# Performance work log

Measured on AMD Instinct MI355X. Metric: run time of the kernel, lower is better.

Reference implementation:

```python
import jax, jax.numpy as jnp
import numpy as np

B, V = 256, 128256

def setup_inputs() -> dict:
    key = jax.random.key(0)
    k1, k2, k3 = jax.random.split(key, 3)
    logits = jax.random.normal(k1, (B, V), dtype=jnp.float32)
    # temperatures in (0, 1.5], with every 8th request greedy (temp == 0)
    u = jax.random.uniform(k2, (B,), dtype=jnp.float32)
    temperatures = jnp.where(jnp.arange(B) % 8 == 0, 0.0, u * 1.4 + 0.1)
    # uniform noise in [0, 1); transformed to Exp(1) inside reference
    noise = jax.random.uniform(k3, (B, V), dtype=jnp.float32)
    return {"logits": logits, "temperatures": temperatures, "noise": noise}

def reference(logits, temperatures, noise):
    logits = logits.astype(jnp.float32)
    greedy_tokens = jnp.argmax(logits, axis=-1)                      # [B]
    scaled = logits / temperatures[:, None]                           # [B, V]
    probs = jax.nn.softmax(scaled, axis=-1)                           # [B, V]
    # torch.empty_like(probs).exponential_(1)  ==  -log(1 - U),  U ~ Uniform[0,1)
    exp_noise = -jnp.log1p(-noise)                                    # Exp(1) noise
    sample_tokens = jnp.argmax(probs / exp_noise, axis=-1)            # Gumbel-max equiv.
    return jnp.where(temperatures == 0, greedy_tokens, sample_tokens)
```

## Files before the change

### kernel.cpp

```cpp
#include <hip/hip_runtime.h>
#include <math.h>


constexpr int TPB = 1024;
constexpr int CHUNKS = 4;

__device__ __forceinline__ void amax_comb(float v, int i, float& bv, int& bi) {
    if (v > bv || (v == bv && i < bi)) { bv = v; bi = i; }
}

__device__ __forceinline__ float gumbel_key(float l, float u, float c) {
    const float w   = 1.0f - u;
    const float enw = __log2f(w) * -0.693147180559945f;
    float p = 0.16666667f;
    p = fmaf(p, u, 0.2f);
    p = fmaf(p, u, 0.25f);
    p = fmaf(p, u, 0.33333333f);
    p = fmaf(p, u, 0.5f);
    p = fmaf(p, u, 1.0f);
    const float en = (u < 0.125f) ? p * u : enw;
    return fmaf(l, c, -__log2f(en));
}

__global__ __launch_bounds__(TPB, 8) void sampler_phase1(
    const float* __restrict__ logits,
    const float* __restrict__ temps,
    const float* __restrict__ noise,
    float* __restrict__ ws_val,
    int* __restrict__ ws_idx, int V)
{
    const int chunk = blockIdx.x & (CHUNKS - 1);
    const int b     = blockIdx.x / CHUNKS;
    const int V4    = V >> 2;
    const int V4c   = V4 / CHUNKS;
    const int gbase = chunk * V4c;
    const float temp = temps[b];
    const float4* __restrict__ lg4 =
        (const float4*)(logits + (size_t)b * V) + gbase;
    const float4* __restrict__ nz4 =
        (const float4*)(noise + (size_t)b * V) + gbase;
    const int t = threadIdx.x;
    const int last = V4c - 1;

    float bv = -INFINITY;
    int   bi = 0x7fffffff;

    if (temp == 0.0f) {
        float4 A = lg4[min(t, last)];
        float4 Bq = lg4[min(t + TPB, last)];
        for (int j = 0; j * TPB < V4c; ++j) {
            const int f = t + j * TPB;
            const float4 l = A;
            A = Bq;
            Bq = lg4[min(f + 2 * TPB, last)];
            if (f < V4c) {
                const int base = (gbase + f) << 2;
                if (l.x > bv) { bv = l.x; bi = base;     }
                if (l.y > bv) { bv = l.y; bi = base + 1; }
                if (l.z > bv) { bv = l.z; bi = base + 2; }
                if (l.w > bv) { bv = l.w; bi = base + 3; }
            }
        }
    } else {
        const float c = (1.0f / temp) * 1.4426950408889634f;
        float4 La = lg4[min(t, last)],       Ua = nz4[min(t, last)];
        float4 Lb = lg4[min(t + TPB, last)], Ub = nz4[min(t + TPB, last)];
        for (int j = 0; j * TPB < V4c; ++j) {
            const int f = t + j * TPB;
            const float4 l = La, u = Ua;
            La = Lb; Ua = Ub;
            const int fn = min(f + 2 * TPB, last);
            Lb = lg4[fn]; Ub = nz4[fn];
            if (f < V4c) {
                const int base = (gbase + f) << 2;
                const float k0 = gumbel_key(l.x, u.x, c);
                const float k1 = gumbel_key(l.y, u.y, c);
                const float k2 = gumbel_key(l.z, u.z, c);
                const float k3 = gumbel_key(l.w, u.w, c);
                if (k0 > bv) { bv = k0; bi = base;     }
                if (k1 > bv) { bv = k1; bi = base + 1; }
                if (k2 > bv) { bv = k2; bi = base + 2; }
                if (k3 > bv) { bv = k3; bi = base + 3; }
            }
        }
    }

    #pragma unroll
    for (int off = 32; off > 0; off >>= 1) {
        const float ov = __shfl_down(bv, off);
        const int   oi = __shfl_down(bi, off);
        amax_comb(ov, oi, bv, bi);
    }

    __shared__ float s_v[TPB / 64];
    __shared__ int   s_i[TPB / 64];
    const int lane = t & 63;
    const int wave = t >> 6;
    if (lane == 0) { s_v[wave] = bv; s_i[wave] = bi; }
    __syncthreads();
    if (t == 0) {
        #pragma unroll
        for (int w = 1; w < TPB / 64; ++w) amax_comb(s_v[w], s_i[w], bv, bi);
        ws_val[blockIdx.x] = bv;
        ws_idx[blockIdx.x] = bi;
    }
}

__global__ void sampler_phase2(const float* __restrict__ ws_val,
                               const int* __restrict__ ws_idx,
                               int* __restrict__ out, int B)
{
    const int b = blockIdx.x * blockDim.x + threadIdx.x;
    if (b >= B) return;
    float bv = -INFINITY;
    int   bi = 0x7fffffff;
    #pragma unroll
    for (int c = 0; c < CHUNKS; ++c) {
        const float v = ws_val[b * CHUNKS + c];
        const int   i = ws_idx[b * CHUNKS + c];
        if (v > bv || (v == bv && i < bi)) { bv = v; bi = i; }
    }
    out[b] = bi;
}

extern "C" void kernel_launch(void* const* d_in, const int* in_sizes, int n_in,
                              void* d_out, int out_size, void* d_ws, size_t ws_size,
                              hipStream_t stream) {
    const float* logits = (const float*)d_in[0];
    const float* temps  = (const float*)d_in[1];
    const float* noise  = (const float*)d_in[2];
    int* out = (int*)d_out;
    const int B = in_sizes[1];
    const int V = in_sizes[0] / B;

    float* ws_val = (float*)d_ws;
    int*   ws_idx = (int*)d_ws + (size_t)B * CHUNKS;

    sampler_phase1<<<B * CHUNKS, TPB, 0, stream>>>(logits, temps, noise,
                                                   ws_val, ws_idx, V);
    sampler_phase2<<<(B + 255) / 256, 256, 0, stream>>>(ws_val, ws_idx, out, B);
}
```

Measured before the change: 272.7 us.

## Deepen load prefetch to three stages with sched barriers and halve block size

Replaces the two-deep software pipeline with a three-deep register rotation, unrolled by four, so more loads are in flight per thread. Scheduling barriers keep the compiler from sinking the prefetch loads past the compute. Block size drops from 1024 to 512, so each thread covers more iterations and more blocks fit per CU. The extra float4 buffers raise register pressure, and iterations past the end now reload clamped addresses.

```diff
diff --git a/kernel.cpp b/kernel.cpp
--- a/kernel.cpp
+++ b/kernel.cpp
@@ -2,7 +2,7 @@
 #include <math.h>
 
 
-constexpr int TPB = 1024;
+constexpr int TPB = 512;
 constexpr int CHUNKS = 4;
 
 __device__ __forceinline__ void amax_comb(float v, int i, float& bv, int& bi) {
@@ -22,6 +22,41 @@
     return fmaf(l, c, -__log2f(en));
 }
 
+#define STEP_S(LI, UI, LC, UC, JI, JC)                                  \
+    {                                                                   \
+        const int fi = min(t + (JI) * TPB, last);                       \
+        LI = lg4[fi];                                                   \
+        UI = nz4[fi];                                                   \
+        __builtin_amdgcn_sched_barrier(0);                              \
+        const int f = t + (JC) * TPB;                                   \
+        if (f < V4c) {                                                  \
+            const int base = (gbase + f) << 2;                          \
+            const float k0 = gumbel_key(LC.x, UC.x, c);                 \
+            const float k1 = gumbel_key(LC.y, UC.y, c);                 \
+            const float k2 = gumbel_key(LC.z, UC.z, c);                 \
+            const float k3 = gumbel_key(LC.w, UC.w, c);                 \
+            if (k0 > bv) { bv = k0; bi = base;     }                    \
+            if (k1 > bv) { bv = k1; bi = base + 1; }                    \
+            if (k2 > bv) { bv = k2; bi = base + 2; }                    \
+            if (k3 > bv) { bv = k3; bi = base + 3; }                    \
+        }                                                               \
+    }
+
+#define STEP_G(LI, LC, JI, JC)                                          \
+    {                                                                   \
+        const int fi = min(t + (JI) * TPB, last);                       \
+        LI = lg4[fi];                                                   \
+        __builtin_amdgcn_sched_barrier(0);                              \
+        const int f = t + (JC) * TPB;                                   \
+        if (f < V4c) {                                                  \
+            const int base = (gbase + f) << 2;                          \
+            if (LC.x > bv) { bv = LC.x; bi = base;     }                \
+            if (LC.y > bv) { bv = LC.y; bi = base + 1; }                \
+            if (LC.z > bv) { bv = LC.z; bi = base + 2; }                \
+            if (LC.w > bv) { bv = LC.w; bi = base + 3; }                \
+        }                                                               \
+    }
+
 __global__ __launch_bounds__(TPB, 8) void sampler_phase1(
     const float* __restrict__ logits,
     const float* __restrict__ temps,
@@ -39,49 +74,36 @@
         (const float4*)(logits + (size_t)b * V) + gbase;
     const float4* __restrict__ nz4 =
         (const float4*)(noise + (size_t)b * V) + gbase;
-    const int t = threadIdx.x;
+    const int t    = threadIdx.x;
     const int last = V4c - 1;
+    const int NIT  = (V4c + TPB - 1) / TPB;
+    const int NIT4 = (NIT + 3) & ~3;
 
     float bv = -INFINITY;
     int   bi = 0x7fffffff;
 
     if (temp == 0.0f) {
-        float4 A = lg4[min(t, last)];
-        float4 Bq = lg4[min(t + TPB, last)];
-        for (int j = 0; j * TPB < V4c; ++j) {
-            const int f = t + j * TPB;
-            const float4 l = A;
-            A = Bq;
-            Bq = lg4[min(f + 2 * TPB, last)];
-            if (f < V4c) {
-                const int base = (gbase + f) << 2;
-                if (l.x > bv) { bv = l.x; bi = base;     }
-                if (l.y > bv) { bv = l.y; bi = base + 1; }
-                if (l.z > bv) { bv = l.z; bi = base + 2; }
-                if (l.w > bv) { bv = l.w; bi = base + 3; }
-            }
+        float4 A0 = lg4[min(t, last)];
+        float4 A1 = lg4[min(t + TPB, last)];
+        float4 A2 = lg4[min(t + 2 * TPB, last)];
+        float4 A3;
+        for (int j = 0; j < NIT4; j += 4) {
+            STEP_G(A3, A0, j + 3, j + 0);
+            STEP_G(A0, A1, j + 4, j + 1);
+            STEP_G(A1, A2, j + 5, j + 2);
+            STEP_G(A2, A3, j + 6, j + 3);
         }
     } else {
         const float c = (1.0f / temp) * 1.4426950408889634f;
-        float4 La = lg4[min(t, last)],       Ua = nz4[min(t, last)];
-        float4 Lb = lg4[min(t + TPB, last)], Ub = nz4[min(t + TPB, last)];
-        for (int j = 0; j * TPB < V4c; ++j) {
-            const int f = t + j * TPB;
-            const float4 l = La, u = Ua;
-            La = Lb; Ua = Ub;
-            const int fn = min(f + 2 * TPB, last);
-            Lb = lg4[fn]; Ub = nz4[fn];
-            if (f < V4c) {
-                const int base = (gbase + f) << 2;
-                const float k0 = gumbel_key(l.x, u.x, c);
-                const float k1 = gumbel_key(l.y, u.y, c);
-                const float k2 = gumbel_key(l.z, u.z, c);
-                const float k3 = gumbel_key(l.w, u.w, c);
-                if (k0 > bv) { bv = k0; bi = base;     }
-                if (k1 > bv) { bv = k1; bi = base + 1; }
-                if (k2 > bv) { bv = k2; bi = base + 2; }
-                if (k3 > bv) { bv = k3; bi = base + 3; }
-            }
+        float4 L0 = lg4[min(t, last)],           U0 = nz4[min(t, last)];
+        float4 L1 = lg4[min(t + TPB, last)],     U1 = nz4[min(t + TPB, last)];
+        float4 L2 = lg4[min(t + 2 * TPB, last)], U2 = nz4[min(t + 2 * TPB, last)];
+        float4 L3, U3;
+        for (int j = 0; j < NIT4; j += 4) {
+            STEP_S(L3, U3, L0, U0, j + 3, j + 0);
+            STEP_S(L0, U0, L1, U1, j + 4, j + 1);
+            STEP_S(L1, U1, L2, U2, j + 5, j + 2);
+            STEP_S(L2, U2, L3, U3, j + 6, j + 3);
         }
     }
 
```

Result: no change. 273.8 us (+0.4%).

## Stream logits and noise through LDS via async global_load_lds pipeline

Applied to the files above, without the earlier changes.

Replaces register-prefetched float4 loads with per-wave asynchronous global-to-LDS loads (global_load_lds, 16 bytes per lane), multi-buffered in shared memory and synchronised with explicit vmcnt waits. The greedy path keeps three loads in flight and the sampling path two stages for both logits and noise. Block size drops from 1024 to 512 threads, so each wave walks a strided set of 64-element segments. The aim is deeper memory-level parallelism with less register pressure on a bandwidth-bound scan, at the cost of fragile hand-placed waitcnt and scheduling barriers, plus extra LDS use that may limit occupancy.

```diff
diff --git a/kernel.cpp b/kernel.cpp
--- a/kernel.cpp
+++ b/kernel.cpp
@@ -2,8 +2,11 @@
 #include <math.h>
 
 
-constexpr int TPB = 1024;
+constexpr int TPB    = 512;
 constexpr int CHUNKS = 4;
+constexpr int WPB    = TPB / 64;
+
+typedef float v4f __attribute__((ext_vector_type(4)));
 
 __device__ __forceinline__ void amax_comb(float v, int i, float& bv, int& bi) {
     if (v > bv || (v == bv && i < bi)) { bv = v; bi = i; }
@@ -22,6 +25,10 @@
     return fmaf(l, c, -__log2f(en));
 }
 
+#define WAITV(N)                                                        \
+    asm volatile("s_waitcnt vmcnt(" #N ")" ::: "memory");               \
+    __builtin_amdgcn_sched_barrier(0)
+
 __global__ __launch_bounds__(TPB, 8) void sampler_phase1(
     const float* __restrict__ logits,
     const float* __restrict__ temps,
@@ -35,24 +42,43 @@
     const int V4c   = V4 / CHUNKS;
     const int gbase = chunk * V4c;
     const float temp = temps[b];
-    const float4* __restrict__ lg4 =
-        (const float4*)(logits + (size_t)b * V) + gbase;
-    const float4* __restrict__ nz4 =
-        (const float4*)(noise + (size_t)b * V) + gbase;
-    const int t = threadIdx.x;
+    const v4f* __restrict__ lg4 =
+        (const v4f*)(logits + (size_t)b * V) + gbase;
+    const v4f* __restrict__ nz4 =
+        (const v4f*)(noise + (size_t)b * V) + gbase;
+    const int t    = threadIdx.x;
+    const int lane = t & 63;
+    const int wave = t >> 6;
     const int last = V4c - 1;
+    const int S_tot = (V4c + 63) >> 6;
+    const int kcnt  = (S_tot - wave + WPB - 1) / WPB;
+
+    __shared__ v4f bufA[2][WPB][64];
+    __shared__ v4f bufB[2][WPB][64];
 
     float bv = -INFINITY;
     int   bi = 0x7fffffff;
 
     if (temp == 0.0f) {
-        float4 A = lg4[min(t, last)];
-        float4 Bq = lg4[min(t + TPB, last)];
-        for (int j = 0; j * TPB < V4c; ++j) {
-            const int f = t + j * TPB;
-            const float4 l = A;
-            A = Bq;
-            Bq = lg4[min(f + 2 * TPB, last)];
+#define G_PTR(B4) ((B4) < 2 ? &bufA[(B4)][wave][0] : &bufB[(B4) - 2][wave][0])
+#define G_ISSUE(K)                                                      \
+        {                                                               \
+            const int s_ = min(wave + WPB * (K), S_tot - 1);            \
+            const int f_ = min(s_ * 64 + lane, last);                   \
+            __builtin_amdgcn_global_load_lds((const void*)(lg4 + f_),   \
+                                             (void*)G_PTR((K) & 3),     \
+                                             16, 0, 0);                 \
+        }
+        G_ISSUE(0); G_ISSUE(1); G_ISSUE(2);
+        for (int k = 0; k < kcnt; ++k) {
+            WAITV(3);
+            const int s = wave + WPB * k;
+            volatile const v4f* p =
+                ((volatile const v4f*)G_PTR(k & 3)) + lane;
+            const v4f l = *p;
+            __builtin_amdgcn_sched_barrier(0);
+            G_ISSUE(k + 3);
+            const int f = s * 64 + lane;
             if (f < V4c) {
                 const int base = (gbase + f) << 2;
                 if (l.x > bv) { bv = l.x; bi = base;     }
@@ -61,16 +87,33 @@
                 if (l.w > bv) { bv = l.w; bi = base + 3; }
             }
         }
+        asm volatile("s_waitcnt vmcnt(0)" ::: "memory");
     } else {
         const float c = (1.0f / temp) * 1.4426950408889634f;
-        float4 La = lg4[min(t, last)],       Ua = nz4[min(t, last)];
-        float4 Lb = lg4[min(t + TPB, last)], Ub = nz4[min(t + TPB, last)];
-        for (int j = 0; j * TPB < V4c; ++j) {
-            const int f = t + j * TPB;
-            const float4 l = La, u = Ua;
-            La = Lb; Ua = Ub;
-            const int fn = min(f + 2 * TPB, last);
-            Lb = lg4[fn]; Ub = nz4[fn];
+#define S_ISSUE(K)                                                      \
+        {                                                               \
+            const int s_ = min(wave + WPB * (K), S_tot - 1);            \
+            const int f_ = min(s_ * 64 + lane, last);                   \
+            const int b_ = (K) & 1;                                     \
+            __builtin_amdgcn_global_load_lds((const void*)(lg4 + f_),   \
+                                             (void*)&bufA[b_][wave][0], \
+                                             16, 0, 0);                 \
+            __builtin_amdgcn_global_load_lds((const void*)(nz4 + f_),   \
+                                             (void*)&bufB[b_][wave][0], \
+                                             16, 0, 0);                 \
+        }
+        S_ISSUE(0); S_ISSUE(1);
+        for (int k = 0; k < kcnt; ++k) {
+            WAITV(2);
+            const int s  = wave + WPB * k;
+            const int b_ = k & 1;
+            volatile const v4f* pL = &bufA[b_][wave][lane];
+            volatile const v4f* pU = &bufB[b_][wave][lane];
+            const v4f l = *pL;
+            const v4f u = *pU;
+            __builtin_amdgcn_sched_barrier(0);
+            S_ISSUE(k + 2);
+            const int f = s * 64 + lane;
             if (f < V4c) {
                 const int base = (gbase + f) << 2;
                 const float k0 = gumbel_key(l.x, u.x, c);
@@ -83,6 +126,7 @@
                 if (k3 > bv) { bv = k3; bi = base + 3; }
             }
         }
+        asm volatile("s_waitcnt vmcnt(0)" ::: "memory");
     }
 
     #pragma unroll
@@ -92,15 +136,13 @@
         amax_comb(ov, oi, bv, bi);
     }
 
-    __shared__ float s_v[TPB / 64];
-    __shared__ int   s_i[TPB / 64];
-    const int lane = t & 63;
-    const int wave = t >> 6;
+    __shared__ float s_v[WPB];
+    __shared__ int   s_i[WPB];
     if (lane == 0) { s_v[wave] = bv; s_i[wave] = bi; }
     __syncthreads();
     if (t == 0) {
         #pragma unroll
-        for (int w = 1; w < TPB / 64; ++w) amax_comb(s_v[w], s_i[w], bv, bi);
+        for (int w = 1; w < WPB; ++w) amax_comb(s_v[w], s_i[w], bv, bi);
         ws_val[blockIdx.x] = bv;
         ws_idx[blockIdx.x] = bi;
     }
```

New measurement: 276.8 us. About the same (+1.5%).

## Use smaller blocks, more chunks, and nontemporal loads unrolled by two

Applied to the files above, without the earlier changes.

Shrinks blocks from 1024 to 256 threads and raises chunks per row from 4 to 8, giving more, smaller blocks for better occupancy and tail balance. The explicit software-prefetch pipeline is replaced by a loop that issues two vector loads per tensor per iteration. Loads now use nontemporal builtins to avoid polluting cache with streamed data. The risk is lost latency hiding from the removed prefetch, and nontemporal hints may change memory throughput in either direction.

```diff
diff --git a/kernel.cpp b/kernel.cpp
--- a/kernel.cpp
+++ b/kernel.cpp
@@ -2,8 +2,10 @@
 #include <math.h>
 
 
-constexpr int TPB = 1024;
-constexpr int CHUNKS = 4;
+constexpr int TPB    = 256;
+constexpr int CHUNKS = 8;
+
+typedef float v4f __attribute__((ext_vector_type(4)));
 
 __device__ __forceinline__ void amax_comb(float v, int i, float& bv, int& bi) {
     if (v > bv || (v == bv && i < bi)) { bv = v; bi = i; }
@@ -35,48 +37,64 @@
     const int V4c   = V4 / CHUNKS;
     const int gbase = chunk * V4c;
     const float temp = temps[b];
-    const float4* __restrict__ lg4 =
-        (const float4*)(logits + (size_t)b * V) + gbase;
-    const float4* __restrict__ nz4 =
-        (const float4*)(noise + (size_t)b * V) + gbase;
-    const int t = threadIdx.x;
+    const v4f* __restrict__ lg4 =
+        (const v4f*)(logits + (size_t)b * V) + gbase;
+    const v4f* __restrict__ nz4 =
+        (const v4f*)(noise + (size_t)b * V) + gbase;
+    const int t    = threadIdx.x;
     const int last = V4c - 1;
+    const int NIT  = (V4c + 2 * TPB - 1) / (2 * TPB);
 
     float bv = -INFINITY;
     int   bi = 0x7fffffff;
 
     if (temp == 0.0f) {
-        float4 A = lg4[min(t, last)];
-        float4 Bq = lg4[min(t + TPB, last)];
-        for (int j = 0; j * TPB < V4c; ++j) {
-            const int f = t + j * TPB;
-            const float4 l = A;
-            A = Bq;
-            Bq = lg4[min(f + 2 * TPB, last)];
-            if (f < V4c) {
-                const int base = (gbase + f) << 2;
-                if (l.x > bv) { bv = l.x; bi = base;     }
-                if (l.y > bv) { bv = l.y; bi = base + 1; }
-                if (l.z > bv) { bv = l.z; bi = base + 2; }
-                if (l.w > bv) { bv = l.w; bi = base + 3; }
+        for (int j = 0; j < NIT; ++j) {
+            const int f0 = t + j * (2 * TPB);
+            const int f1 = f0 + TPB;
+            const v4f a = __builtin_nontemporal_load(lg4 + min(f0, last));
+            const v4f bq = __builtin_nontemporal_load(lg4 + min(f1, last));
+            if (f0 < V4c) {
+                const int base = (gbase + f0) << 2;
+                if (a.x > bv) { bv = a.x; bi = base;     }
+                if (a.y > bv) { bv = a.y; bi = base + 1; }
+                if (a.z > bv) { bv = a.z; bi = base + 2; }
+                if (a.w > bv) { bv = a.w; bi = base + 3; }
+            }
+            if (f1 < V4c) {
+                const int base = (gbase + f1) << 2;
+                if (bq.x > bv) { bv = bq.x; bi = base;     }
+                if (bq.y > bv) { bv = bq.y; bi = base + 1; }
+                if (bq.z > bv) { bv = bq.z; bi = base + 2; }
+                if (bq.w > bv) { bv = bq.w; bi = base + 3; }
             }
         }
     } else {
         const float c = (1.0f / temp) * 1.4426950408889634f;
-        float4 La = lg4[min(t, last)],       Ua = nz4[min(t, last)];
-        float4 Lb = lg4[min(t + TPB, last)], Ub = nz4[min(t + TPB, last)];
-        for (int j = 0; j * TPB < V4c; ++j) {
-            const int f = t + j * TPB;
-            const float4 l = La, u = Ua;
-            La = Lb; Ua = Ub;
-            const int fn = min(f + 2 * TPB, last);
-            Lb = lg4[fn]; Ub = nz4[fn];
-            if (f < V4c) {
-                const int base = (gbase + f) << 2;
-                const float k0 = gumbel_key(l.x, u.x, c);
-                const float k1 = gumbel_key(l.y, u.y, c);
-                const float k2 = gumbel_key(l.z, u.z, c);
-                const float k3 = gumbel_key(l.w, u.w, c);
+        for (int j = 0; j < NIT; ++j) {
+            const int f0 = t + j * (2 * TPB);
+            const int f1 = f0 + TPB;
+            const v4f l0 = __builtin_nontemporal_load(lg4 + min(f0, last));
+            const v4f u0 = __builtin_nontemporal_load(nz4 + min(f0, last));
+            const v4f l1 = __builtin_nontemporal_load(lg4 + min(f1, last));
+            const v4f u1 = __builtin_nontemporal_load(nz4 + min(f1, last));
+            if (f0 < V4c) {
+                const int base = (gbase + f0) << 2;
+                const float k0 = gumbel_key(l0.x, u0.x, c);
+                const float k1 = gumbel_key(l0.y, u0.y, c);
+                const float k2 = gumbel_key(l0.z, u0.z, c);
+                const float k3 = gumbel_key(l0.w, u0.w, c);
+                if (k0 > bv) { bv = k0; bi = base;     }
+                if (k1 > bv) { bv = k1; bi = base + 1; }
+                if (k2 > bv) { bv = k2; bi = base + 2; }
+                if (k3 > bv) { bv = k3; bi = base + 3; }
+            }
+            if (f1 < V4c) {
+                const int base = (gbase + f1) << 2;
+                const float k0 = gumbel_key(l1.x, u1.x, c);
+                const float k1 = gumbel_key(l1.y, u1.y, c);
+                const float k2 = gumbel_key(l1.z, u1.z, c);
+                const float k3 = gumbel_key(l1.w, u1.w, c);
                 if (k0 > bv) { bv = k0; bi = base;     }
                 if (k1 > bv) { bv = k1; bi = base + 1; }
                 if (k2 > bv) { bv = k2; bi = base + 2; }
```

Result: faster. 248.0 us (-9.1%).
